# Kernel tuning notes

Measured on AMD Instinct MI355X. Metric: run time of the kernel, lower is better.

The kernel has to match this reference:

```python
import jax, jax.numpy as jnp
import numpy as np

NUM_USERS = 60000
NUM_ITEMS = 40000
N_NODES = NUM_USERS + NUM_ITEMS
EMBED_K = 128
E_HALF = 1_000_000  # bipartite interactions; symmetrized -> 2M directed edges


def setup_inputs() -> dict:
    key = jax.random.key(0)
    k1, k2, k3, k4, k5, k6, k7 = jax.random.split(key, 7)
    scale = 1.0 / np.sqrt(EMBED_K)  # ~ xavier_normal
    Gu = jax.random.normal(k1, (NUM_USERS, EMBED_K), jnp.float32) * scale
    Gi = jax.random.normal(k2, (NUM_ITEMS, EMBED_K), jnp.float32) * scale
    W0 = jax.random.normal(k3, (EMBED_K, EMBED_K), jnp.float32) * scale
    W1 = jax.random.normal(k4, (EMBED_K, EMBED_K), jnp.float32) * scale
    W2 = jax.random.normal(k5, (EMBED_K, EMBED_K), jnp.float32) * scale
    # bipartite user-item graph, symmetrized (items offset by NUM_USERS)
    u = jax.random.randint(k6, (E_HALF,), 0, NUM_USERS)
    it = jax.random.randint(k7, (E_HALF,), 0, NUM_ITEMS) + NUM_USERS
    src = jnp.concatenate([u, it])
    dst = jnp.concatenate([it, u])
    edge_index = jnp.stack([src, dst]).astype(jnp.int32)  # [2, 2M]
    return {"Gu": Gu, "Gi": Gi, "W0": W0, "W1": W1, "W2": W2,
            "edge_index": edge_index}


def reference(Gu, Gi, W0, W1, W2, edge_index):
    # add_self_loops=False, bias=False) -> ReLU), then split into (gu, gi).
    src, dst = edge_index[0], edge_index[1]
    n_users = Gu.shape[0]
    n_nodes = Gu.shape[0] + Gi.shape[0]
    # PyG gcn_norm (no self loops): deg = scatter(1, col); norm = d^-1/2[row]*d^-1/2[col]
    ones = jnp.ones(src.shape, Gu.dtype)
    deg = jax.ops.segment_sum(ones, dst, num_segments=n_nodes)
    dinv = jnp.where(deg > 0, jax.lax.rsqrt(jnp.maximum(deg, 1.0)), 0.0)
    norm = dinv[src] * dinv[dst]  # [E]
    x = jnp.concatenate([Gu, Gi], axis=0)  # [N, d]
    for W in (W0, W1, W2):
        h = x @ W                                   # [N, d] dense GEMM
        msg = h[src] * norm[:, None]                # [E, d] gather + scale
        x = jax.nn.relu(jax.ops.segment_sum(msg, dst, num_segments=n_nodes))
    return x[:n_users], x[n_users:]
```

## Files before the change

### kernel.cpp

```cpp
#include <hip/hip_runtime.h>
#include <hip/hip_bf16.h>

#define EMB 128
#define NPB 256
#define NB_PAD 512
#define CHUNK 4096

typedef unsigned int uint32;
typedef __attribute__((ext_vector_type(8))) short bf16x8;
typedef __attribute__((ext_vector_type(4))) float f32x4;

__device__ __forceinline__ ushort f2bf(float f) {
    uint32 u = __float_as_uint(f);
    return (ushort)((u + 0x7fff + ((u >> 16) & 1)) >> 16);
}
__device__ __forceinline__ uint32 pack_hi2(uint32 u0, uint32 u1) {
    return (u1 & 0xffff0000u) | (u0 >> 16);
}


__global__ __launch_bounds__(256) void bucket_count_kernel(
    const int* __restrict__ dst, int* __restrict__ bucket_cnt, int E, int NB) {
    __shared__ int cnt[NB_PAD];
    int t = threadIdx.x;
    long e0 = (long)blockIdx.x * CHUNK;
    int n = E - (int)e0; if (n > CHUNK) n = CHUNK;
    for (int b = t; b < NB_PAD; b += 256) cnt[b] = 0;
    __syncthreads();
    #pragma unroll
    for (int i = 0; i < CHUNK / 256; i++) {
        int idx = t + i * 256;
        if (idx < n) atomicAdd(&cnt[dst[e0 + idx] >> 8], 1);
    }
    __syncthreads();
    for (int b = t; b < NB; b += 256)
        if (cnt[b] > 0) atomicAdd(&bucket_cnt[b], cnt[b]);
}

__global__ void bucket_scan_kernel(const int* __restrict__ bucket_cnt,
                                   int* __restrict__ ebase, int* __restrict__ gcursor,
                                   int NB, int E) {
    __shared__ int sc[512];
    int t = threadIdx.x;
    int v = (t < NB) ? bucket_cnt[t] : 0;
    sc[t] = v;
    __syncthreads();
    for (int off = 1; off < 512; off <<= 1) {
        int u = (t >= off) ? sc[t - off] : 0;
        __syncthreads();
        sc[t] += u;
        __syncthreads();
    }
    if (t < NB) {
        int excl = sc[t] - v;
        ebase[t] = excl;
        gcursor[t] = excl;
    }
    if (t == 0) ebase[NB] = E;
}


__global__ __launch_bounds__(256) void bucket_scatter_kernel(
    const int* __restrict__ src, const int* __restrict__ dst,
    int* __restrict__ gcursor, uint2* __restrict__ ebuf, int E, int NB) {
    __shared__ int cnt[NB_PAD];
    __shared__ int loff[NB_PAD];
    __shared__ int gbase[NB_PAD];
    __shared__ int pos[NB_PAD];
    __shared__ int sc[256];
    __shared__ uint2 stage[CHUNK];
    int t = threadIdx.x;
    long e0 = (long)blockIdx.x * CHUNK;
    int n = E - (int)e0; if (n > CHUNK) n = CHUNK;
    for (int b = t; b < NB_PAD; b += 256) { cnt[b] = 0; pos[b] = 0; }
    __syncthreads();
    int es[CHUNK / 256], ed[CHUNK / 256];
    #pragma unroll
    for (int i = 0; i < CHUNK / 256; i++) {
        int idx = t + i * 256;
        if (idx < n) {
            es[i] = src[e0 + idx];
            ed[i] = dst[e0 + idx];
            atomicAdd(&cnt[ed[i] >> 8], 1);
        }
    }
    __syncthreads();
    int a = cnt[2 * t], b2 = cnt[2 * t + 1];
    sc[t] = a + b2;
    __syncthreads();
    for (int off = 1; off < 256; off <<= 1) {
        int v = (t >= off) ? sc[t - off] : 0;
        __syncthreads();
        sc[t] += v;
        __syncthreads();
    }
    int excl = sc[t] - (a + b2);
    loff[2 * t] = excl;
    loff[2 * t + 1] = excl + a;
    __syncthreads();
    for (int b = t; b < NB; b += 256)
        if (cnt[b] > 0) gbase[b] = atomicAdd(&gcursor[b], cnt[b]);
    __syncthreads();
    #pragma unroll
    for (int i = 0; i < CHUNK / 256; i++) {
        int idx = t + i * 256;
        if (idx < n) {
            int b = ed[i] >> 8;
            int p = atomicAdd(&pos[b], 1);
            stage[loff[b] + p] = make_uint2((uint32)es[i], (uint32)ed[i]);
        }
    }
    __syncthreads();
    for (int b = t; b < NB; b += 256) {
        int c = cnt[b], lo = loff[b], go = gbase[b];
        for (int k = 0; k < c; k++) ebuf[go + k] = stage[lo + k];
    }
}


__global__ __launch_bounds__(256) void bucket_deg_kernel(
    const uint2* __restrict__ ebuf, const int* __restrict__ ebase,
    int* __restrict__ deg, float* __restrict__ dinv, int N) {
    __shared__ int cnt[NPB];
    int t = threadIdx.x;
    int n0 = blockIdx.x * NPB;
    int nn = N - n0; if (nn > NPB) nn = NPB;
    cnt[t] = 0;
    __syncthreads();
    int e0 = ebase[blockIdx.x];
    int e1 = ebase[blockIdx.x + 1];
    for (int e = e0 + t; e < e1; e += 256) {
        uint2 sd = ebuf[e];
        atomicAdd(&cnt[(int)sd.y - n0], 1);
    }
    __syncthreads();
    if (t < nn) {
        int c = cnt[t];
        deg[n0 + t] = c;
        dinv[n0 + t] = c > 0 ? rsqrtf((float)c) : 0.0f;
    }
}


__global__ void scan1_kernel(const int* __restrict__ deg, int* __restrict__ rowptr,
                             int* __restrict__ bsum, int N) {
    __shared__ int sc[256];
    int t = threadIdx.x;
    int base = blockIdx.x * 1024 + t * 4;
    int d0 = 0, d1 = 0, d2 = 0, d3 = 0;
    if (base + 3 < N) {
        int4 v = *(const int4*)(deg + base);
        d0 = v.x; d1 = v.y; d2 = v.z; d3 = v.w;
    } else {
        if (base     < N) d0 = deg[base];
        if (base + 1 < N) d1 = deg[base + 1];
        if (base + 2 < N) d2 = deg[base + 2];
        if (base + 3 < N) d3 = deg[base + 3];
    }
    int s = d0 + d1 + d2 + d3;
    sc[t] = s;
    __syncthreads();
    for (int off = 1; off < 256; off <<= 1) {
        int v = (t >= off) ? sc[t - off] : 0;
        __syncthreads();
        sc[t] += v;
        __syncthreads();
    }
    int excl = sc[t] - s;
    if (t == 255) bsum[blockIdx.x] = sc[255];
    int dd[4] = {d0, d1, d2, d3};
    int p = excl;
    #pragma unroll
    for (int j = 0; j < 4; j++) {
        int i = base + j;
        if (i < N) rowptr[i] = p;
        p += dd[j];
    }
}

__global__ void scan2_kernel(int* bsum, int nb) {
    __shared__ int sc[128];
    int t = threadIdx.x;
    int v = (t < nb) ? bsum[t] : 0;
    sc[t] = v;
    __syncthreads();
    for (int off = 1; off < 128; off <<= 1) {
        int u = (t >= off) ? sc[t - off] : 0;
        __syncthreads();
        sc[t] += u;
        __syncthreads();
    }
    if (t < nb) bsum[t] = sc[t] - v;
}

__global__ void scan3_kernel(int* __restrict__ rowptr, const int* __restrict__ bsum,
                             int N, int E) {
    int t = threadIdx.x, b = blockIdx.x;
    int add = bsum[b];
    int base = b * 1024 + t * 4;
    #pragma unroll
    for (int j = 0; j < 4; j++) {
        int i = base + j;
        if (i < N) rowptr[i] += add;
    }
    if (b == 0 && t == 0) rowptr[N] = E;
}


__global__ __launch_bounds__(256) void bucket_fill_kernel(
    const uint2* __restrict__ ebuf, const int* __restrict__ rowptr,
    int* __restrict__ csr, int N) {
    __shared__ int cnt[NPB];
    __shared__ int rp[NPB];
    int t = threadIdx.x;
    int n0 = blockIdx.x * NPB;
    int nn = N - n0; if (nn > NPB) nn = NPB;
    if (t < nn) { cnt[t] = 0; rp[t] = rowptr[n0 + t]; }
    __syncthreads();
    int e0 = rowptr[n0];
    int e1 = rowptr[n0 + nn];
    for (int e = e0 + t; e < e1; e += 256) {
        uint2 sd = ebuf[e];
        int local = (int)sd.y - n0;
        int p = atomicAdd(&cnt[local], 1);
        csr[rp[local] + p] = (int)sd.x;
    }
}


__global__ __launch_bounds__(256) void agg_relu_kernel(
    const uint32* __restrict__ Yh,
    const int* __restrict__ rowptr, const int* __restrict__ csr,
    const float* __restrict__ dinv, float* __restrict__ out, int N) {
    int node = blockIdx.x * 4 + (threadIdx.x >> 6);
    int lane = threadIdx.x & 63;
    if (node >= N) return;
    int e0 = rowptr[node], e1 = rowptr[node + 1];
    float ax = 0.0f, ay = 0.0f;
    for (int base = e0; base < e1; base += 64) {
        int n = e1 - base;
        if (n > 64) n = 64;
        int s = 0;
        float w = 0.0f;
        if (lane < n) {
            s = csr[base + lane];
            w = dinv[s];
        }
        int nn = (n + 15) & ~15;
        for (int j = 0; j < nn; j += 16) {
            uint32 p[16];
            float wj[16];
            #pragma unroll
            for (int u = 0; u < 16; u++) {
                int sj = __shfl(s, j + u);
                wj[u] = __shfl(w, j + u);
                p[u] = Yh[(size_t)sj * 64 + lane];
            }
            #pragma unroll
            for (int u = 0; u < 16; u++) {
                ax += wj[u] * __uint_as_float(p[u] << 16);
                ay += wj[u] * __uint_as_float(p[u] & 0xffff0000u);
            }
        }
    }
    float wd = dinv[node];
    float2 r;
    r.x = fmaxf(ax * wd, 0.0f);
    r.y = fmaxf(ay * wd, 0.0f);
    *(float2*)(out + (size_t)node * EMB + lane * 2) = r;
}


__global__ void wsplit_kernel(const float* __restrict__ W0, const float* __restrict__ W1,
                              const float* __restrict__ W2,
                              ushort* __restrict__ Whi, ushort* __restrict__ Wlo) {
    const float* W = (blockIdx.x == 0) ? W0 : (blockIdx.x == 1) ? W1 : W2;
    ushort* hiT = Whi + blockIdx.x * EMB * EMB;
    ushort* loT = Wlo + blockIdx.x * EMB * EMB;
    for (int i = threadIdx.x; i < EMB * EMB; i += blockDim.x) {
        int k = i >> 7, n = i & 127;
        float w = W[i];
        uint32 u = __float_as_uint(w);
        ushort hi = (ushort)(u >> 16);
        float hif = __uint_as_float(u & 0xffff0000u);
        ushort lo = f2bf(w - hif);
        hiT[n * EMB + k] = hi;
        loT[n * EMB + k] = lo;
    }
}


union FragU { uint32 u[4]; bf16x8 v; };

__global__ __launch_bounds__(256, 2) void gemm_mfma_kernel(
    const float* __restrict__ A, const ushort* __restrict__ WhiT,
    const ushort* __restrict__ WloT, ushort* __restrict__ Yh, int M) {
    __shared__ float As[16][132];
    int t = threadIdx.x;
    int wv = t >> 6, lane = t & 63, quad = lane >> 4, l16 = lane & 15;

    FragU bfr[8][2];
    #pragma unroll
    for (int kc = 0; kc < 8; kc++) {
        const ushort* srcW = (kc < 4) ? WhiT : WloT;
        int kb = (kc & 3) * 32 + quad * 8;
        #pragma unroll
        for (int c = 0; c < 2; c++) {
            int n = wv * 32 + c * 16 + l16;
            const uint32* p = (const uint32*)(srcW + n * EMB + kb);
            bfr[kc][c].u[0] = p[0];
            bfr[kc][c].u[1] = p[1];
            bfr[kc][c].u[2] = p[2];
            bfr[kc][c].u[3] = p[3];
        }
    }

    int srow = t >> 4, skq = t & 15;
    int ntile = (M + 15) >> 4;
    for (int tile = blockIdx.x; tile < ntile; tile += (int)gridDim.x) {
        int r0 = tile << 4;
        __syncthreads();
        {
            float4 v0 = {0.f, 0.f, 0.f, 0.f}, v1 = v0;
            int row = r0 + srow;
            if (row < M) {
                const float* ga = A + (size_t)row * EMB + skq * 8;
                v0 = *(const float4*)ga;
                v1 = *(const float4*)(ga + 4);
            }
            *(float4*)&As[srow][skq * 8] = v0;
            *(float4*)&As[srow][skq * 8 + 4] = v1;
        }
        __syncthreads();

        FragU ah[4], al[4];
        #pragma unroll
        for (int kc = 0; kc < 4; kc++) {
            const float* p = &As[l16][kc * 32 + quad * 8];
            float4 xa = *(const float4*)p;
            float4 xb = *(const float4*)(p + 4);
            uint32 u0 = __float_as_uint(xa.x), u1 = __float_as_uint(xa.y);
            uint32 u2 = __float_as_uint(xa.z), u3 = __float_as_uint(xa.w);
            uint32 u4 = __float_as_uint(xb.x), u5 = __float_as_uint(xb.y);
            uint32 u6 = __float_as_uint(xb.z), u7 = __float_as_uint(xb.w);
            ah[kc].u[0] = pack_hi2(u0, u1);
            ah[kc].u[1] = pack_hi2(u2, u3);
            ah[kc].u[2] = pack_hi2(u4, u5);
            ah[kc].u[3] = pack_hi2(u6, u7);
            float l0 = xa.x - __uint_as_float(u0 & 0xffff0000u);
            float l1 = xa.y - __uint_as_float(u1 & 0xffff0000u);
            float l2 = xa.z - __uint_as_float(u2 & 0xffff0000u);
            float l3 = xa.w - __uint_as_float(u3 & 0xffff0000u);
            float l4 = xb.x - __uint_as_float(u4 & 0xffff0000u);
            float l5 = xb.y - __uint_as_float(u5 & 0xffff0000u);
            float l6 = xb.z - __uint_as_float(u6 & 0xffff0000u);
            float l7 = xb.w - __uint_as_float(u7 & 0xffff0000u);
            al[kc].u[0] = pack_hi2(__float_as_uint(l0), __float_as_uint(l1));
            al[kc].u[1] = pack_hi2(__float_as_uint(l2), __float_as_uint(l3));
            al[kc].u[2] = pack_hi2(__float_as_uint(l4), __float_as_uint(l5));
            al[kc].u[3] = pack_hi2(__float_as_uint(l6), __float_as_uint(l7));
        }

        f32x4 acc0 = {0.f, 0.f, 0.f, 0.f};
        f32x4 acc1 = {0.f, 0.f, 0.f, 0.f};
        #pragma unroll
        for (int kc = 0; kc < 4; kc++) {
            acc0 = __builtin_amdgcn_mfma_f32_16x16x32_bf16(ah[kc].v, bfr[kc][0].v, acc0, 0, 0, 0);
            acc1 = __builtin_amdgcn_mfma_f32_16x16x32_bf16(ah[kc].v, bfr[kc][1].v, acc1, 0, 0, 0);
        }
        #pragma unroll
        for (int kc = 0; kc < 4; kc++) {
            acc0 = __builtin_amdgcn_mfma_f32_16x16x32_bf16(ah[kc].v, bfr[kc + 4][0].v, acc0, 0, 0, 0);
            acc1 = __builtin_amdgcn_mfma_f32_16x16x32_bf16(ah[kc].v, bfr[kc + 4][1].v, acc1, 0, 0, 0);
        }
        #pragma unroll
        for (int kc = 0; kc < 4; kc++) {
            acc0 = __builtin_amdgcn_mfma_f32_16x16x32_bf16(al[kc].v, bfr[kc][0].v, acc0, 0, 0, 0);
            acc1 = __builtin_amdgcn_mfma_f32_16x16x32_bf16(al[kc].v, bfr[kc][1].v, acc1, 0, 0, 0);
        }

        int colb = wv * 32 + l16;
        #pragma unroll
        for (int r = 0; r < 4; r++) {
            int row = r0 + quad * 4 + r;
            if (row < M) {
                Yh[(size_t)row * EMB + colb]      = f2bf(acc0[r]);
                Yh[(size_t)row * EMB + colb + 16] = f2bf(acc1[r]);
            }
        }
    }
}


extern "C" void kernel_launch(void* const* d_in, const int* in_sizes, int n_in,
                              void* d_out, int out_size, void* d_ws, size_t ws_size,
                              hipStream_t stream) {
    (void)n_in; (void)out_size; (void)ws_size;
    const float* Gu = (const float*)d_in[0];
    const float* Gi = (const float*)d_in[1];
    const float* W0 = (const float*)d_in[2];
    const float* W1 = (const float*)d_in[3];
    const float* W2 = (const float*)d_in[4];
    const int* ei = (const int*)d_in[5];

    int nu = in_sizes[0] / EMB;
    int ni = in_sizes[1] / EMB;
    int N = nu + ni;
    int E = in_sizes[5] / 2;
    const int* src = ei;
    const int* dst = ei + E;
    int NB = (N + NPB - 1) / NPB;

    ushort* Yh      = (ushort*)d_ws;
    uint2* ebuf     = (uint2*)(Yh + (size_t)N * EMB);
    int* deg        = (int*)(ebuf + (size_t)E);
    int* rowptr     = deg + N;
    float* dinv     = (float*)(rowptr + N + 1);
    int* csr        = (int*)(dinv + N);
    int* bucket_cnt = csr + E;
    int* ebase      = bucket_cnt + NB;
    int* gcursor    = ebase + NB + 1;
    int* bsum       = gcursor + NB;
    ushort* WhiT    = (ushort*)(bsum + 128);
    ushort* WloT    = WhiT + 3 * EMB * EMB;
    float* X        = (float*)d_out;

    hipMemsetAsync(bucket_cnt, 0, sizeof(int) * (size_t)NB, stream);

    wsplit_kernel<<<3, 256, 0, stream>>>(W0, W1, W2, WhiT, WloT);

    int ecb = (E + CHUNK - 1) / CHUNK;
    bucket_count_kernel<<<ecb, 256, 0, stream>>>(dst, bucket_cnt, E, NB);
    bucket_scan_kernel<<<1, 512, 0, stream>>>(bucket_cnt, ebase, gcursor, NB, E);
    bucket_scatter_kernel<<<ecb, 256, 0, stream>>>(src, dst, gcursor, ebuf, E, NB);
    bucket_deg_kernel<<<NB, 256, 0, stream>>>(ebuf, ebase, deg, dinv, N);
    int nb = (N + 1023) / 1024;
    scan1_kernel<<<nb, 256, 0, stream>>>(deg, rowptr, bsum, N);
    scan2_kernel<<<1, 128, 0, stream>>>(bsum, nb);
    scan3_kernel<<<nb, 256, 0, stream>>>(rowptr, bsum, N, E);
    bucket_fill_kernel<<<NB, 256, 0, stream>>>(ebuf, rowptr, csr, N);

    int aggBlocks = (N + 3) / 4;
    const int GB = 512;

    gemm_mfma_kernel<<<GB, 256, 0, stream>>>(Gu, WhiT, WloT, Yh, nu);
    gemm_mfma_kernel<<<GB, 256, 0, stream>>>(Gi, WhiT, WloT, Yh + (size_t)nu * EMB, ni);
    agg_relu_kernel<<<aggBlocks, 256, 0, stream>>>((const uint32*)Yh, rowptr, csr, dinv, X, N);
    gemm_mfma_kernel<<<GB, 256, 0, stream>>>(X, WhiT + EMB * EMB, WloT + EMB * EMB, Yh, N);
    agg_relu_kernel<<<aggBlocks, 256, 0, stream>>>((const uint32*)Yh, rowptr, csr, dinv, X, N);
    gemm_mfma_kernel<<<GB, 256, 0, stream>>>(X, WhiT + 2 * EMB * EMB, WloT + 2 * EMB * EMB, Yh, N);
    agg_relu_kernel<<<aggBlocks, 256, 0, stream>>>((const uint32*)Yh, rowptr, csr, dinv, X, N);
}
```

Measured before the change: 472.2 us.

## Pack neighbor index with source weight and restructure aggregation into 16-lane groups

```diff
diff --git a/kernel.cpp b/kernel.cpp
--- a/kernel.cpp
+++ b/kernel.cpp
@@ -5,8 +5,10 @@
 #define NPB 256
 #define NB_PAD 512
 #define CHUNK 4096
+#define FILL_CAP 7168
 
 typedef unsigned int uint32;
+typedef unsigned long long uint64;
 typedef __attribute__((ext_vector_type(8))) short bf16x8;
 typedef __attribute__((ext_vector_type(4))) float f32x4;
 
@@ -17,6 +19,8 @@
 __device__ __forceinline__ uint32 pack_hi2(uint32 u0, uint32 u1) {
     return (u1 & 0xffff0000u) | (u0 >> 16);
 }
+__device__ __forceinline__ float blo(uint32 u) { return __uint_as_float(u << 16); }
+__device__ __forceinline__ float bhi(uint32 u) { return __uint_as_float(u & 0xffff0000u); }
 
 
 __global__ __launch_bounds__(256) void bucket_count_kernel(
@@ -207,9 +211,10 @@
 }
 
 
-__global__ __launch_bounds__(256) void bucket_fill_kernel(
-    const uint2* __restrict__ ebuf, const int* __restrict__ rowptr,
-    int* __restrict__ csr, int N) {
+__global__ __launch_bounds__(256) void fill_ew_kernel(
+    uint2* __restrict__ ebuf, const int* __restrict__ rowptr,
+    const float* __restrict__ dinv, int N) {
+    __shared__ uint2 stage[FILL_CAP];
     __shared__ int cnt[NPB];
     __shared__ int rp[NPB];
     int t = threadIdx.x;
@@ -219,55 +224,81 @@
     __syncthreads();
     int e0 = rowptr[n0];
     int e1 = rowptr[n0 + nn];
-    for (int e = e0 + t; e < e1; e += 256) {
-        uint2 sd = ebuf[e];
+    int ecount = e1 - e0; if (ecount > FILL_CAP) ecount = FILL_CAP;
+    for (int o = t; o < ecount; o += 256) stage[o] = ebuf[e0 + o];
+    __syncthreads();
+    for (int o = t; o < ecount; o += 256) {
+        uint2 sd = stage[o];
         int local = (int)sd.y - n0;
         int p = atomicAdd(&cnt[local], 1);
-        csr[rp[local] + p] = (int)sd.x;
-    }
-}
-
+        int s = (int)sd.x;
+        ebuf[rp[local] + p] = make_uint2((uint32)s, __float_as_uint(dinv[s]));
+    }
+}
+
+
+#define ACC8(P, W) do { \
+    a0 += (W) * blo((P).x); a1 += (W) * bhi((P).x); \
+    a2 += (W) * blo((P).y); a3 += (W) * bhi((P).y); \
+    a4 += (W) * blo((P).z); a5 += (W) * bhi((P).z); \
+    a6 += (W) * blo((P).w); a7 += (W) * bhi((P).w); } while (0)
 
 __global__ __launch_bounds__(256) void agg_relu_kernel(
     const uint32* __restrict__ Yh,
-    const int* __restrict__ rowptr, const int* __restrict__ csr,
+    const int* __restrict__ rowptr, const uint2* __restrict__ ew,
     const float* __restrict__ dinv, float* __restrict__ out, int N) {
     int node = blockIdx.x * 4 + (threadIdx.x >> 6);
+    if (node >= N) return;
     int lane = threadIdx.x & 63;
-    if (node >= N) return;
+    int grp = lane >> 4, l4 = lane & 15;
     int e0 = rowptr[node], e1 = rowptr[node + 1];
-    float ax = 0.0f, ay = 0.0f;
-    for (int base = e0; base < e1; base += 64) {
-        int n = e1 - base;
-        if (n > 64) n = 64;
-        int s = 0;
-        float w = 0.0f;
-        if (lane < n) {
-            s = csr[base + lane];
-            w = dinv[s];
-        }
-        int nn = (n + 15) & ~15;
-        for (int j = 0; j < nn; j += 16) {
-            uint32 p[16];
-            float wj[16];
-            #pragma unroll
-            for (int u = 0; u < 16; u++) {
-                int sj = __shfl(s, j + u);
-                wj[u] = __shfl(w, j + u);
-                p[u] = Yh[(size_t)sj * 64 + lane];
-            }
-            #pragma unroll
-            for (int u = 0; u < 16; u++) {
-                ax += wj[u] * __uint_as_float(p[u] << 16);
-                ay += wj[u] * __uint_as_float(p[u] & 0xffff0000u);
-            }
-        }
-    }
-    float wd = dinv[node];
-    float2 r;
-    r.x = fmaxf(ax * wd, 0.0f);
-    r.y = fmaxf(ay * wd, 0.0f);
-    *(float2*)(out + (size_t)node * EMB + lane * 2) = r;
+    float a0 = 0.f, a1 = 0.f, a2 = 0.f, a3 = 0.f;
+    float a4 = 0.f, a5 = 0.f, a6 = 0.f, a7 = 0.f;
+    if (e0 < e1) {
+        int eA0 = e0 + grp, eA1 = e0 + 4 + grp;
+        int ecA0 = eA0 < e1 ? eA0 : e0;
+        int ecA1 = eA1 < e1 ? eA1 : e0;
+        uint64 mv0 = __builtin_nontemporal_load((const uint64*)(ew + ecA0));
+        uint64 mv1 = __builtin_nontemporal_load((const uint64*)(ew + ecA1));
+        float wA0 = eA0 < e1 ? __uint_as_float((uint32)(mv0 >> 32)) : 0.0f;
+        float wA1 = eA1 < e1 ? __uint_as_float((uint32)(mv1 >> 32)) : 0.0f;
+        uint4 pA0 = *(const uint4*)(Yh + (size_t)(uint32)mv0 * 64 + l4 * 4);
+        uint4 pA1 = *(const uint4*)(Yh + (size_t)(uint32)mv1 * 64 + l4 * 4);
+        for (int base = e0 + 8; base < e1; base += 8) {
+            int eB0 = base + grp, eB1 = base + 4 + grp;
+            int ecB0 = eB0 < e1 ? eB0 : e0;
+            int ecB1 = eB1 < e1 ? eB1 : e0;
+            uint64 nv0 = __builtin_nontemporal_load((const uint64*)(ew + ecB0));
+            uint64 nv1 = __builtin_nontemporal_load((const uint64*)(ew + ecB1));
+            float wB0 = eB0 < e1 ? __uint_as_float((uint32)(nv0 >> 32)) : 0.0f;
+            float wB1 = eB1 < e1 ? __uint_as_float((uint32)(nv1 >> 32)) : 0.0f;
+            uint4 pB0 = *(const uint4*)(Yh + (size_t)(uint32)nv0 * 64 + l4 * 4);
+            uint4 pB1 = *(const uint4*)(Yh + (size_t)(uint32)nv1 * 64 + l4 * 4);
+            ACC8(pA0, wA0);
+            ACC8(pA1, wA1);
+            pA0 = pB0; pA1 = pB1; wA0 = wB0; wA1 = wB1;
+        }
+        ACC8(pA0, wA0);
+        ACC8(pA1, wA1);
+    }
+    a0 += __shfl_xor(a0, 16); a0 += __shfl_xor(a0, 32);
+    a1 += __shfl_xor(a1, 16); a1 += __shfl_xor(a1, 32);
+    a2 += __shfl_xor(a2, 16); a2 += __shfl_xor(a2, 32);
+    a3 += __shfl_xor(a3, 16); a3 += __shfl_xor(a3, 32);
+    a4 += __shfl_xor(a4, 16); a4 += __shfl_xor(a4, 32);
+    a5 += __shfl_xor(a5, 16); a5 += __shfl_xor(a5, 32);
+    a6 += __shfl_xor(a6, 16); a6 += __shfl_xor(a6, 32);
+    a7 += __shfl_xor(a7, 16); a7 += __shfl_xor(a7, 32);
+    if (grp == 0) {
+        float wd = dinv[node];
+        f32x4 r0 = { fmaxf(a0 * wd, 0.f), fmaxf(a1 * wd, 0.f),
+                     fmaxf(a2 * wd, 0.f), fmaxf(a3 * wd, 0.f) };
+        f32x4 r1 = { fmaxf(a4 * wd, 0.f), fmaxf(a5 * wd, 0.f),
+                     fmaxf(a6 * wd, 0.f), fmaxf(a7 * wd, 0.f) };
+        float* po = out + (size_t)node * EMB + l4 * 8;
+        __builtin_nontemporal_store(r0, (f32x4*)po);
+        __builtin_nontemporal_store(r1, (f32x4*)(po + 4));
+    }
 }
 
 
@@ -293,8 +324,9 @@
 union FragU { uint32 u[4]; bf16x8 v; };
 
 __global__ __launch_bounds__(256, 2) void gemm_mfma_kernel(
-    const float* __restrict__ A, const ushort* __restrict__ WhiT,
-    const ushort* __restrict__ WloT, ushort* __restrict__ Yh, int M) {
+    const float* __restrict__ A, const float* __restrict__ A2, int Msplit,
+    const ushort* __restrict__ WhiT, const ushort* __restrict__ WloT,
+    ushort* __restrict__ Yh, int M) {
     __shared__ float As[16][132];
     int t = threadIdx.x;
     int wv = t >> 6, lane = t & 63, quad = lane >> 4, l16 = lane & 15;
@@ -324,7 +356,9 @@
             float4 v0 = {0.f, 0.f, 0.f, 0.f}, v1 = v0;
             int row = r0 + srow;
             if (row < M) {
-                const float* ga = A + (size_t)row * EMB + skq * 8;
+                const float* ga = (row < Msplit)
+                    ? A  + (size_t)row * EMB + skq * 8
+                    : A2 + (size_t)(row - Msplit) * EMB + skq * 8;
                 v0 = *(const float4*)ga;
                 v1 = *(const float4*)(ga + 4);
             }
@@ -416,8 +450,7 @@
     int* deg        = (int*)(ebuf + (size_t)E);
     int* rowptr     = deg + N;
     float* dinv     = (float*)(rowptr + N + 1);
-    int* csr        = (int*)(dinv + N);
-    int* bucket_cnt = csr + E;
+    int* bucket_cnt = (int*)(dinv + N);
     int* ebase      = bucket_cnt + NB;
     int* gcursor    = ebase + NB + 1;
     int* bsum       = gcursor + NB;
@@ -438,16 +471,16 @@
     scan1_kernel<<<nb, 256, 0, stream>>>(deg, rowptr, bsum, N);
     scan2_kernel<<<1, 128, 0, stream>>>(bsum, nb);
     scan3_kernel<<<nb, 256, 0, stream>>>(rowptr, bsum, N, E);
-    bucket_fill_kernel<<<NB, 256, 0, stream>>>(ebuf, rowptr, csr, N);
-
+    fill_ew_kernel<<<NB, 256, 0, stream>>>(ebuf, rowptr, dinv, N);
+
+    const uint2* ew = (const uint2*)ebuf;
     int aggBlocks = (N + 3) / 4;
     const int GB = 512;
 
-    gemm_mfma_kernel<<<GB, 256, 0, stream>>>(Gu, WhiT, WloT, Yh, nu);
-    gemm_mfma_kernel<<<GB, 256, 0, stream>>>(Gi, WhiT, WloT, Yh + (size_t)nu * EMB, ni);
-    agg_relu_kernel<<<aggBlocks, 256, 0, stream>>>((const uint32*)Yh, rowptr, csr, dinv, X, N);
-    gemm_mfma_kernel<<<GB, 256, 0, stream>>>(X, WhiT + EMB * EMB, WloT + EMB * EMB, Yh, N);
-    agg_relu_kernel<<<aggBlocks, 256, 0, stream>>>((const uint32*)Yh, rowptr, csr, dinv, X, N);
-    gemm_mfma_kernel<<<GB, 256, 0, stream>>>(X, WhiT + 2 * EMB * EMB, WloT + 2 * EMB * EMB, Yh, N);
-    agg_relu_kernel<<<aggBlocks, 256, 0, stream>>>((const uint32*)Yh, rowptr, csr, dinv, X, N);
-}
+    gemm_mfma_kernel<<<GB, 256, 0, stream>>>(Gu, Gi, nu, WhiT, WloT, Yh, N);
+    agg_relu_kernel<<<aggBlocks, 256, 0, stream>>>((const uint32*)Yh, rowptr, ew, dinv, X, N);
+    gemm_mfma_kernel<<<GB, 256, 0, stream>>>(X, X, N, WhiT + EMB * EMB, WloT + EMB * EMB, Yh, N);
+    agg_relu_kernel<<<aggBlocks, 256, 0, stream>>>((const uint32*)Yh, rowptr, ew, dinv, X, N);
+    gemm_mfma_kernel<<<GB, 256, 0, stream>>>(X, X, N, WhiT + 2 * EMB * EMB, WloT + 2 * EMB * EMB, Yh, N);
+    agg_relu_kernel<<<aggBlocks, 256, 0, stream>>>((const uint32*)Yh, rowptr, ew, dinv, X, N);
+}
```

Measured after the change: 509.1 us. +7.8%, slower.
